# Kernel optimization log

Hardware: AMD Instinct MI355X
Metric: run time of the kernel (lower is better)

Reference implementation:

```python
import jax, jax.numpy as jnp
import numpy as np

E = 100000
VERTEX_DIM = 64
EDGE_DIM = 128
MESSAGE_DIM = 64


def setup_inputs() -> dict:
    key = jax.random.key(0)
    k1, k2, k3, k4 = jax.random.split(key, 4)
    vertices = jax.random.normal(k1, (E, VERTEX_DIM), dtype=jnp.float32)
    edges = jax.random.normal(k2, (E, EDGE_DIM), dtype=jnp.float32)
    # nn.Linear(edge_dim, message_dim * vertex_dim): weight [out, in], bias [out]
    W = jax.random.normal(k3, (MESSAGE_DIM * VERTEX_DIM, EDGE_DIM), dtype=jnp.float32) * (1.0 / np.sqrt(EDGE_DIM))
    b = jax.random.normal(k4, (MESSAGE_DIM * VERTEX_DIM,), dtype=jnp.float32) * 0.01
    return {"vertices": vertices, "edges": edges, "W": W, "b": b}


def reference(vertices, edges, W, b):
    # edge_net(edges): [E, message_dim*vertex_dim]
    proj = edges @ W.T + b
    # view to [E, message_dim, vertex_dim], then batched matvec with vertices [E, vertex_dim]
    proj = proj.reshape(edges.shape[0], MESSAGE_DIM, VERTEX_DIM)
    message = jnp.einsum('emv,ev->em', proj, vertices)  # [E, message_dim]
    return message
```

## Files before the change

kernel.cpp:

```cpp
#include <hip/hip_runtime.h>
#include <hip/hip_bf16.h>
#include <stdint.h>


typedef _Float16 f16;
typedef __attribute__((ext_vector_type(2))) _Float16 f16x2;
typedef __attribute__((ext_vector_type(8))) _Float16 f16x8;
typedef __attribute__((ext_vector_type(4))) float f32x4;

#define MSG_D 64
#define VTX_D 64
#define EDG_D 128

__device__ __forceinline__ f16x8 cvt8(float4 a, float4 d) {
  return (f16x8){(f16)a.x, (f16)a.y, (f16)a.z, (f16)a.w,
                 (f16)d.x, (f16)d.y, (f16)d.z, (f16)d.w};
}

__global__ void prep_w(const float* __restrict__ W, const float* __restrict__ b,
                       f16* __restrict__ Wh, f16* __restrict__ Bh) {
  int tid = blockIdx.x * 256 + threadIdx.x;
  if (tid < 65536) {
    int L = tid & 63, n = (tid >> 6) & 3, s = (tid >> 8) & 3, v = tid >> 10;
    int q = L >> 4, ln = L & 15;
    const float* src = W + (size_t)((n * 16 + ln) * 64 + v) * 128 + s * 32 + q * 8;
    float4 a = *(const float4*)src, d = *(const float4*)(src + 4);
    *(f16x8*)(Wh + (size_t)tid * 8) = cvt8(a, d);
  } else if (tid < 66048) {
    int t2 = tid - 65536;
    int L = t2 & 63, n = (t2 >> 6) & 3, s2 = t2 >> 8;
    int q = L >> 4, ln = L & 15;
    const float* src = b + (n * 16 + ln) * 64 + s2 * 32 + q * 8;
    float4 a = *(const float4*)src, d = *(const float4*)(src + 4);
    *(f16x8*)(Bh + (size_t)t2 * 8) = cvt8(a, d);
  }
}

__global__ __launch_bounds__(64, 2) void edge_msg_flat(
    const float* __restrict__ Vtx, const float* __restrict__ Xe,
    const f16* __restrict__ Wh, const f16* __restrict__ Bh,
    float* __restrict__ out, int E)
{
  const int lane = threadIdx.x;
  const int q = lane >> 4, ln = lane & 15;
  const int eoff = blockIdx.x * 64;

  int er[4];
  f16x8 xh[4][4];
  #pragma unroll
  for (int t = 0; t < 4; ++t) {
    int e = eoff + 16 * t + ln;
    er[t] = e < E ? e : E - 1;
    const float* xr = Xe + (size_t)er[t] * EDG_D;
    #pragma unroll
    for (int s = 0; s < 4; ++s) {
      float4 a = *(const float4*)(xr + s * 32 + q * 8);
      float4 d = *(const float4*)(xr + s * 32 + q * 8 + 4);
      xh[t][s] = cvt8(a, d);
    }
  }

  f32x4 acc[4][4];
  #pragma unroll
  for (int t = 0; t < 4; ++t)
    #pragma unroll
    for (int n = 0; n < 4; ++n) acc[t][n] = (f32x4){0.f, 0.f, 0.f, 0.f};

  const f16* wp = Wh + (size_t)lane * 8;

  f16x8 wA[8], wB[8];
  #pragma unroll
  for (int c = 0; c < 8; ++c) wA[c] = *(const f16x8*)(wp + c * 512);

  f16x8 vrow[4];
  #pragma unroll
  for (int t = 0; t < 4; ++t) {
    const float* vsrc = Vtx + (size_t)er[t] * VTX_D;
    float4 a = *(const float4*)(vsrc), d = *(const float4*)(vsrc + 4);
    vrow[t] = cvt8(a, d);
  }

  #pragma unroll 1
  for (int c8 = 0; c8 < 8; ++c8) {
    f16x8 vnext[4];
    if (c8 < 7) {
      #pragma unroll
      for (int t = 0; t < 4; ++t) {
        const float* vsrc = Vtx + (size_t)er[t] * VTX_D + (c8 + 1) * 8;
        float4 a = *(const float4*)(vsrc), d = *(const float4*)(vsrc + 4);
        vnext[t] = cvt8(a, d);
      }
    }

    #pragma unroll
    for (int j = 0; j < 8; ++j) {
      const int v = c8 * 8 + j;
      const f16* wrow  = wp + (size_t)v * 8192;
      const f16* wrowN = wp + (size_t)(v < 63 ? v + 1 : 63) * 8192;

      #pragma unroll
      for (int c = 0; c < 8; ++c) wB[c] = *(const f16x8*)(wrow + (8 + c) * 512);

      f16x2 hv[4];
      #pragma unroll
      for (int t = 0; t < 4; ++t) { f16 h = vrow[t][j]; hv[t] = (f16x2){h, h}; }

      #pragma unroll
      for (int s = 0; s < 2; ++s) {
        f16x8 af[4];
        #pragma unroll
        for (int t = 0; t < 4; ++t) {
          union { f16x8 v8; f16x2 h2[4]; } x, r;
          x.v8 = xh[t][s];
          r.h2[0] = hv[t] * x.h2[0];
          r.h2[1] = hv[t] * x.h2[1];
          r.h2[2] = hv[t] * x.h2[2];
          r.h2[3] = hv[t] * x.h2[3];
          af[t] = r.v8;
        }
        #pragma unroll
        for (int n = 0; n < 4; ++n)
          #pragma unroll
          for (int t = 0; t < 4; ++t)
            acc[t][n] = __builtin_amdgcn_mfma_f32_16x16x32_f16(af[t], wA[s * 4 + n], acc[t][n], 0, 0, 0);
      }

      #pragma unroll
      for (int c = 0; c < 8; ++c) wA[c] = *(const f16x8*)(wrowN + c * 512);

      #pragma unroll
      for (int s = 2; s < 4; ++s) {
        f16x8 af[4];
        #pragma unroll
        for (int t = 0; t < 4; ++t) {
          union { f16x8 v8; f16x2 h2[4]; } x, r;
          x.v8 = xh[t][s];
          r.h2[0] = hv[t] * x.h2[0];
          r.h2[1] = hv[t] * x.h2[1];
          r.h2[2] = hv[t] * x.h2[2];
          r.h2[3] = hv[t] * x.h2[3];
          af[t] = r.v8;
        }
        #pragma unroll
        for (int n = 0; n < 4; ++n)
          #pragma unroll
          for (int t = 0; t < 4; ++t)
            acc[t][n] = __builtin_amdgcn_mfma_f32_16x16x32_f16(af[t], wB[(s - 2) * 4 + n], acc[t][n], 0, 0, 0);
      }
    }

    #pragma unroll
    for (int t = 0; t < 4; ++t) vrow[t] = vnext[t];
  }

  #pragma unroll
  for (int s2 = 0; s2 < 2; ++s2) {
    f16x8 av[4];
    #pragma unroll
    for (int t = 0; t < 4; ++t) {
      const float* vr2 = Vtx + (size_t)er[t] * VTX_D + s2 * 32 + q * 8;
      float4 a = *(const float4*)vr2, d = *(const float4*)(vr2 + 4);
      av[t] = cvt8(a, d);
    }
    #pragma unroll
    for (int n = 0; n < 4; ++n) {
      f16x8 bf = *(const f16x8*)(Bh + (size_t)((s2 * 4 + n) * 64 + lane) * 8);
      #pragma unroll
      for (int t = 0; t < 4; ++t)
        acc[t][n] = __builtin_amdgcn_mfma_f32_16x16x32_f16(av[t], bf, acc[t][n], 0, 0, 0);
    }
  }

  #pragma unroll
  for (int t = 0; t < 4; ++t)
    #pragma unroll
    for (int r = 0; r < 4; ++r) {
      int e = eoff + 16 * t + 4 * q + r;
      if (e < E) {
        float* orow = out + (size_t)e * MSG_D;
        #pragma unroll
        for (int n = 0; n < 4; ++n) orow[n * 16 + ln] = acc[t][n][r];
      }
    }
}

__global__ void edge_msg_naive(const float* __restrict__ Vtx, const float* __restrict__ Xe,
                               const float* __restrict__ W, const float* __restrict__ b,
                               float* __restrict__ out, int E) {
  __shared__ float xs[EDG_D];
  __shared__ float vs[VTX_D];
  int e = blockIdx.x;
  int m = threadIdx.x;
  for (int i = m; i < EDG_D; i += 64) xs[i] = Xe[(size_t)e * EDG_D + i];
  for (int i = m; i < VTX_D; i += 64) vs[i] = Vtx[(size_t)e * VTX_D + i];
  __syncthreads();
  float s = 0.f;
  for (int v = 0; v < VTX_D; ++v) {
    const float* wr = W + (size_t)(m * 64 + v) * EDG_D;
    float p = b[m * 64 + v];
    for (int k = 0; k < EDG_D; ++k) p += xs[k] * wr[k];
    s += p * vs[v];
  }
  out[(size_t)e * MSG_D + m] = s;
}

extern "C" void kernel_launch(void* const* d_in, const int* in_sizes, int n_in,
                              void* d_out, int out_size, void* d_ws, size_t ws_size,
                              hipStream_t stream) {
  const float* Vtx = (const float*)d_in[0];
  const float* Xe  = (const float*)d_in[1];
  const float* W   = (const float*)d_in[2];
  const float* b   = (const float*)d_in[3];
  float* out = (float*)d_out;

  const int E  = in_sizes[0] / VTX_D;
  const int nW = in_sizes[2];
  const int nb = in_sizes[3];

  const size_t needW = (size_t)(524288 + 4096) * sizeof(f16);

  if (nW != 524288 || nb != 4096 || ws_size < needW) {
    edge_msg_naive<<<E, 64, 0, stream>>>(Vtx, Xe, W, b, out, E);
    return;
  }

  f16* Wh = (f16*)d_ws;
  f16* Bh = Wh + 524288;

  prep_w<<<258, 256, 0, stream>>>(W, b, Wh, Bh);

  int blocks = (E + 63) / 64;
  edge_msg_flat<<<blocks, 64, 0, stream>>>(Vtx, Xe, Wh, Bh, out, E);
}
```

Before: 247.2 us.

## Stage W slices in LDS via async triple-buffered loads shared by four waves

Each block grows from one to four waves covering 256 edges. The per-v W slices are streamed into a three-slot LDS ring with global_load_lds, so one slice serves all four waves instead of each wave loading W from global into registers. Vertex values are transposed into LDS as f16 once per block, replacing repeated global reloads. This cuts global/L2 traffic for W and frees registers, but adds a block barrier every v step plus LDS read traffic.

```diff
diff --git a/kernel.cpp b/kernel.cpp
--- a/kernel.cpp
+++ b/kernel.cpp
@@ -1,5 +1,4 @@
 #include <hip/hip_runtime.h>
-#include <hip/hip_bf16.h>
 #include <stdint.h>
 
 
@@ -36,14 +35,25 @@
   }
 }
 
-__global__ __launch_bounds__(64, 2) void edge_msg_flat(
+typedef __attribute__((address_space(1))) const void GV;
+typedef __attribute__((address_space(3))) void LV;
+__device__ __forceinline__ void gload_lds16(const void* g, void* l) {
+  __builtin_amdgcn_global_load_lds((GV*)g, (LV*)l, 16, 0, 0);
+}
+
+__global__ __launch_bounds__(256, 2) void edge_msg_lds(
     const float* __restrict__ Vtx, const float* __restrict__ Xe,
     const f16* __restrict__ Wh, const f16* __restrict__ Bh,
     float* __restrict__ out, int E)
 {
-  const int lane = threadIdx.x;
+  __shared__ f16 Wsh[3 * 8192];
+  __shared__ f16 Vt[64 * 256];
+
+  const int tid = threadIdx.x;
+  const int wid = tid >> 6, lane = tid & 63;
   const int q = lane >> 4, ln = lane & 15;
-  const int eoff = blockIdx.x * 64;
+  const int eblk = blockIdx.x * 256;
+  const int eoff = eblk + wid * 64;
 
   int er[4];
   f16x8 xh[4][4];
@@ -60,97 +70,93 @@
     }
   }
 
+  {
+    int e = eblk + tid;
+    int ec = e < E ? e : E - 1;
+    const float* vr = Vtx + (size_t)ec * VTX_D;
+    #pragma unroll
+    for (int k = 0; k < 16; ++k) {
+      float4 a = *(const float4*)(vr + k * 4);
+      Vt[(k * 4 + 0) * 256 + tid] = (f16)a.x;
+      Vt[(k * 4 + 1) * 256 + tid] = (f16)a.y;
+      Vt[(k * 4 + 2) * 256 + tid] = (f16)a.z;
+      Vt[(k * 4 + 3) * 256 + tid] = (f16)a.w;
+    }
+  }
+
   f32x4 acc[4][4];
   #pragma unroll
   for (int t = 0; t < 4; ++t)
     #pragma unroll
     for (int n = 0; n < 4; ++n) acc[t][n] = (f32x4){0.f, 0.f, 0.f, 0.f};
 
-  const f16* wp = Wh + (size_t)lane * 8;
-
-  f16x8 wA[8], wB[8];
-  #pragma unroll
-  for (int c = 0; c < 8; ++c) wA[c] = *(const f16x8*)(wp + c * 512);
-
-  f16x8 vrow[4];
-  #pragma unroll
-  for (int t = 0; t < 4; ++t) {
-    const float* vsrc = Vtx + (size_t)er[t] * VTX_D;
-    float4 a = *(const float4*)(vsrc), d = *(const float4*)(vsrc + 4);
-    vrow[t] = cvt8(a, d);
-  }
+  asm volatile("s_waitcnt lgkmcnt(0)" ::: "memory");
+  __builtin_amdgcn_s_barrier();
+  asm volatile("" ::: "memory");
+
+  {
+    const char* gbase = (const char*)Wh + (size_t)(wid * 4) * 1024 + (size_t)lane * 16;
+    char* lbase = (char*)&Wsh[0] + (wid * 4) * 1024;
+    #pragma unroll
+    for (int c = 0; c < 4; ++c) gload_lds16(gbase + c * 1024, lbase + c * 1024);
+    #pragma unroll
+    for (int c = 0; c < 4; ++c)
+      gload_lds16(gbase + 16384 + c * 1024, lbase + 2 * 8192 + c * 1024);
+  }
+
+  int bo = 0;
 
   #pragma unroll 1
-  for (int c8 = 0; c8 < 8; ++c8) {
-    f16x8 vnext[4];
-    if (c8 < 7) {
+  for (int v = 0; v < 64; ++v) {
+    if (v == 63) asm volatile("s_waitcnt vmcnt(0)" ::: "memory");
+    else         asm volatile("s_waitcnt vmcnt(4)" ::: "memory");
+    __builtin_amdgcn_s_barrier();
+    asm volatile("" ::: "memory");
+
+    if (v < 62) {
+      int so = bo + 2 * 8192;
+      if (so >= 3 * 8192) so -= 3 * 8192;
+      const char* gbase = (const char*)Wh + (size_t)(v + 2) * 16384 +
+                          (size_t)(wid * 4) * 1024 + (size_t)lane * 16;
+      char* lbase = (char*)&Wsh[so] + (wid * 4) * 1024;
+      #pragma unroll
+      for (int c = 0; c < 4; ++c) gload_lds16(gbase + c * 1024, lbase + c * 1024);
+    }
+
+    f16x2 hv[4];
+    #pragma unroll
+    for (int t = 0; t < 4; ++t) {
+      f16 h = Vt[v * 256 + wid * 64 + 16 * t + ln];
+      hv[t] = (f16x2){h, h};
+    }
+
+    const f16* wb = &Wsh[bo + lane * 8];
+    #pragma unroll
+    for (int s = 0; s < 4; ++s) {
+      f16x8 bf[4];
+      #pragma unroll
+      for (int n = 0; n < 4; ++n) bf[n] = *(const f16x8*)(wb + (s * 4 + n) * 512);
+
+      f16x8 af[4];
       #pragma unroll
       for (int t = 0; t < 4; ++t) {
-        const float* vsrc = Vtx + (size_t)er[t] * VTX_D + (c8 + 1) * 8;
-        float4 a = *(const float4*)(vsrc), d = *(const float4*)(vsrc + 4);
-        vnext[t] = cvt8(a, d);
+        union { f16x8 v8; f16x2 h2[4]; } x, r;
+        x.v8 = xh[t][s];
+        r.h2[0] = hv[t] * x.h2[0];
+        r.h2[1] = hv[t] * x.h2[1];
+        r.h2[2] = hv[t] * x.h2[2];
+        r.h2[3] = hv[t] * x.h2[3];
+        af[t] = r.v8;
       }
-    }
-
-    #pragma unroll
-    for (int j = 0; j < 8; ++j) {
-      const int v = c8 * 8 + j;
-      const f16* wrow  = wp + (size_t)v * 8192;
-      const f16* wrowN = wp + (size_t)(v < 63 ? v + 1 : 63) * 8192;
-
-      #pragma unroll
-      for (int c = 0; c < 8; ++c) wB[c] = *(const f16x8*)(wrow + (8 + c) * 512);
-
-      f16x2 hv[4];
-      #pragma unroll
-      for (int t = 0; t < 4; ++t) { f16 h = vrow[t][j]; hv[t] = (f16x2){h, h}; }
-
-      #pragma unroll
-      for (int s = 0; s < 2; ++s) {
-        f16x8 af[4];
+      #pragma unroll
+      for (int n = 0; n < 4; ++n)
         #pragma unroll
-        for (int t = 0; t < 4; ++t) {
-          union { f16x8 v8; f16x2 h2[4]; } x, r;
-          x.v8 = xh[t][s];
-          r.h2[0] = hv[t] * x.h2[0];
-          r.h2[1] = hv[t] * x.h2[1];
-          r.h2[2] = hv[t] * x.h2[2];
-          r.h2[3] = hv[t] * x.h2[3];
-          af[t] = r.v8;
-        }
-        #pragma unroll
-        for (int n = 0; n < 4; ++n)
-          #pragma unroll
-          for (int t = 0; t < 4; ++t)
-            acc[t][n] = __builtin_amdgcn_mfma_f32_16x16x32_f16(af[t], wA[s * 4 + n], acc[t][n], 0, 0, 0);
-      }
-
-      #pragma unroll
-      for (int c = 0; c < 8; ++c) wA[c] = *(const f16x8*)(wrowN + c * 512);
-
-      #pragma unroll
-      for (int s = 2; s < 4; ++s) {
-        f16x8 af[4];
-        #pragma unroll
-        for (int t = 0; t < 4; ++t) {
-          union { f16x8 v8; f16x2 h2[4]; } x, r;
-          x.v8 = xh[t][s];
-          r.h2[0] = hv[t] * x.h2[0];
-          r.h2[1] = hv[t] * x.h2[1];
-          r.h2[2] = hv[t] * x.h2[2];
-          r.h2[3] = hv[t] * x.h2[3];
-          af[t] = r.v8;
-        }
-        #pragma unroll
-        for (int n = 0; n < 4; ++n)
-          #pragma unroll
-          for (int t = 0; t < 4; ++t)
-            acc[t][n] = __builtin_amdgcn_mfma_f32_16x16x32_f16(af[t], wB[(s - 2) * 4 + n], acc[t][n], 0, 0, 0);
-      }
-    }
-
-    #pragma unroll
-    for (int t = 0; t < 4; ++t) vrow[t] = vnext[t];
+        for (int t = 0; t < 4; ++t)
+          acc[t][n] = __builtin_amdgcn_mfma_f32_16x16x32_f16(af[t], bf[n], acc[t][n], 0, 0, 0);
+    }
+
+    bo += 8192;
+    if (bo >= 3 * 8192) bo -= 3 * 8192;
   }
 
   #pragma unroll
@@ -164,10 +170,10 @@
     }
     #pragma unroll
     for (int n = 0; n < 4; ++n) {
-      f16x8 bf = *(const f16x8*)(Bh + (size_t)((s2 * 4 + n) * 64 + lane) * 8);
+      f16x8 bfb = *(const f16x8*)(Bh + (size_t)((s2 * 4 + n) * 64 + lane) * 8);
       #pragma unroll
       for (int t = 0; t < 4; ++t)
-        acc[t][n] = __builtin_amdgcn_mfma_f32_16x16x32_f16(av[t], bf, acc[t][n], 0, 0, 0);
+        acc[t][n] = __builtin_amdgcn_mfma_f32_16x16x32_f16(av[t], bfb, acc[t][n], 0, 0, 0);
     }
   }
 
@@ -229,6 +235,6 @@
 
   prep_w<<<258, 256, 0, stream>>>(W, b, Wh, Bh);
 
-  int blocks = (E + 63) / 64;
-  edge_msg_flat<<<blocks, 64, 0, stream>>>(Vtx, Xe, Wh, Bh, out, E);
-}
+  int blocks = (E + 255) / 256;
+  edge_msg_lds<<<blocks, 256, 0, stream>>>(Vtx, Xe, Wh, Bh, out, E);
+}
```

Result: faster. 206.0 us (-16.7%).

## Stage fp16 weights through an LDS ring shared by three waves

Applied to the files above, without the earlier changes.

Replaces each wave's register-prefetch of the fp16 weight slice from global memory with a 5-slot LDS ring buffer. The ring is filled asynchronously by global_load_lds across a 3-wave block, and the waves synchronise with manual vmcnt waits and barriers. Each weight slice is fetched from global or L2 once per block instead of once per wave, cutting L2 traffic. The cost is a barrier per v-step, LDS read pressure and fragile hand-tuned vmcnt counts.

```diff
diff --git a/kernel.cpp b/kernel.cpp
--- a/kernel.cpp
+++ b/kernel.cpp
@@ -1,5 +1,4 @@
 #include <hip/hip_runtime.h>
-#include <hip/hip_bf16.h>
 #include <stdint.h>
 
 
@@ -36,14 +35,23 @@
   }
 }
 
-__global__ __launch_bounds__(64, 2) void edge_msg_flat(
+typedef __attribute__((address_space(1))) const void GV;
+typedef __attribute__((address_space(3))) void LV;
+__device__ __forceinline__ void gload_lds16(const void* g, void* l) {
+  __builtin_amdgcn_global_load_lds((GV*)g, (LV*)l, 16, 0, 0);
+}
+
+__global__ __launch_bounds__(192, 2) void edge_msg_lds(
     const float* __restrict__ Vtx, const float* __restrict__ Xe,
     const f16* __restrict__ Wh, const f16* __restrict__ Bh,
     float* __restrict__ out, int E)
 {
-  const int lane = threadIdx.x;
+  __shared__ f16 Wring[5 * 8192];
+
+  const int tid = threadIdx.x;
+  const int wid = tid >> 6, lane = tid & 63;
   const int q = lane >> 4, ln = lane & 15;
-  const int eoff = blockIdx.x * 64;
+  const int eoff = blockIdx.x * 192 + wid * 64;
 
   int er[4];
   f16x8 xh[4][4];
@@ -60,18 +68,6 @@
     }
   }
 
-  f32x4 acc[4][4];
-  #pragma unroll
-  for (int t = 0; t < 4; ++t)
-    #pragma unroll
-    for (int n = 0; n < 4; ++n) acc[t][n] = (f32x4){0.f, 0.f, 0.f, 0.f};
-
-  const f16* wp = Wh + (size_t)lane * 8;
-
-  f16x8 wA[8], wB[8];
-  #pragma unroll
-  for (int c = 0; c < 8; ++c) wA[c] = *(const f16x8*)(wp + c * 512);
-
   f16x8 vrow[4];
   #pragma unroll
   for (int t = 0; t < 4; ++t) {
@@ -80,33 +76,81 @@
     vrow[t] = cvt8(a, d);
   }
 
+  f32x4 acc[4][4];
+  #pragma unroll
+  for (int t = 0; t < 4; ++t)
+    #pragma unroll
+    for (int n = 0; n < 4; ++n) acc[t][n] = (f32x4){0.f, 0.f, 0.f, 0.f};
+
+  {
+    const char* gb = (const char*)Wh + (size_t)lane * 16;
+    #pragma unroll
+    for (int v = 0; v < 4; ++v) {
+      char* lb = (char*)Wring + (size_t)v * 16384;
+      #pragma unroll
+      for (int k = 0; k < 6; ++k) {
+        int g = wid + 3 * k;
+        if (g < 16) gload_lds16(gb + (size_t)v * 16384 + g * 1024, lb + g * 1024);
+      }
+    }
+  }
+
+  int cur = 0;
+  int st  = 4;
+
   #pragma unroll 1
   for (int c8 = 0; c8 < 8; ++c8) {
-    f16x8 vnext[4];
-    if (c8 < 7) {
-      #pragma unroll
-      for (int t = 0; t < 4; ++t) {
-        const float* vsrc = Vtx + (size_t)er[t] * VTX_D + (c8 + 1) * 8;
-        float4 a = *(const float4*)(vsrc), d = *(const float4*)(vsrc + 4);
-        vnext[t] = cvt8(a, d);
-      }
-    }
+    float4 vna[4], vnd[4];
 
     #pragma unroll
     for (int j = 0; j < 8; ++j) {
-      const int v = c8 * 8 + j;
-      const f16* wrow  = wp + (size_t)v * 8192;
-      const f16* wrowN = wp + (size_t)(v < 63 ? v + 1 : 63) * 8192;
-
-      #pragma unroll
-      for (int c = 0; c < 8; ++c) wB[c] = *(const f16x8*)(wrow + (8 + c) * 512);
+      const int i = c8 * 8 + j;
+
+      if (i < 61) {
+        if (wid == 0) asm volatile("s_waitcnt vmcnt(18)" ::: "memory");
+        else          asm volatile("s_waitcnt vmcnt(15)" ::: "memory");
+      } else if (i == 61) {
+        if (wid == 0) asm volatile("s_waitcnt vmcnt(12)" ::: "memory");
+        else          asm volatile("s_waitcnt vmcnt(10)" ::: "memory");
+      } else if (i == 62) {
+        if (wid == 0) asm volatile("s_waitcnt vmcnt(6)" ::: "memory");
+        else          asm volatile("s_waitcnt vmcnt(5)" ::: "memory");
+      } else {
+        asm volatile("s_waitcnt vmcnt(0)" ::: "memory");
+      }
+      __builtin_amdgcn_s_barrier();
+      asm volatile("" ::: "memory");
+
+      if (i < 60) {
+        const char* gb = (const char*)Wh + (size_t)(i + 4) * 16384 + (size_t)lane * 16;
+        char* lb = (char*)Wring + (size_t)st * 16384;
+        #pragma unroll
+        for (int k = 0; k < 6; ++k) {
+          int g = wid + 3 * k;
+          if (g < 16) gload_lds16(gb + g * 1024, lb + g * 1024);
+        }
+      }
+
+      if (j == 6 && c8 < 7) {
+        #pragma unroll
+        for (int t = 0; t < 4; ++t) {
+          const float* vsrc = Vtx + (size_t)er[t] * VTX_D + (c8 + 1) * 8;
+          vna[t] = *(const float4*)(vsrc);
+          vnd[t] = *(const float4*)(vsrc + 4);
+        }
+      }
 
       f16x2 hv[4];
       #pragma unroll
       for (int t = 0; t < 4; ++t) { f16 h = vrow[t][j]; hv[t] = (f16x2){h, h}; }
 
-      #pragma unroll
-      for (int s = 0; s < 2; ++s) {
+      const f16* wb = Wring + (size_t)cur * 8192 + lane * 8;
+      #pragma unroll
+      for (int s = 0; s < 4; ++s) {
+        f16x8 bf[4];
+        #pragma unroll
+        for (int n = 0; n < 4; ++n) bf[n] = *(const f16x8*)(wb + (s * 4 + n) * 512);
+
         f16x8 af[4];
         #pragma unroll
         for (int t = 0; t < 4; ++t) {
@@ -122,35 +166,17 @@
         for (int n = 0; n < 4; ++n)
           #pragma unroll
           for (int t = 0; t < 4; ++t)
-            acc[t][n] = __builtin_amdgcn_mfma_f32_16x16x32_f16(af[t], wA[s * 4 + n], acc[t][n], 0, 0, 0);
-      }
-
-      #pragma unroll
-      for (int c = 0; c < 8; ++c) wA[c] = *(const f16x8*)(wrowN + c * 512);
-
-      #pragma unroll
-      for (int s = 2; s < 4; ++s) {
-        f16x8 af[4];
-        #pragma unroll
-        for (int t = 0; t < 4; ++t) {
-          union { f16x8 v8; f16x2 h2[4]; } x, r;
-          x.v8 = xh[t][s];
-          r.h2[0] = hv[t] * x.h2[0];
-          r.h2[1] = hv[t] * x.h2[1];
-          r.h2[2] = hv[t] * x.h2[2];
-          r.h2[3] = hv[t] * x.h2[3];
-          af[t] = r.v8;
-        }
-        #pragma unroll
-        for (int n = 0; n < 4; ++n)
-          #pragma unroll
-          for (int t = 0; t < 4; ++t)
-            acc[t][n] = __builtin_amdgcn_mfma_f32_16x16x32_f16(af[t], wB[(s - 2) * 4 + n], acc[t][n], 0, 0, 0);
-      }
-    }
-
-    #pragma unroll
-    for (int t = 0; t < 4; ++t) vrow[t] = vnext[t];
+            acc[t][n] = __builtin_amdgcn_mfma_f32_16x16x32_f16(af[t], bf[n], acc[t][n], 0, 0, 0);
+      }
+
+      cur = (cur == 4) ? 0 : cur + 1;
+      st  = (st  == 4) ? 0 : st  + 1;
+    }
+
+    if (c8 < 7) {
+      #pragma unroll
+      for (int t = 0; t < 4; ++t) vrow[t] = cvt8(vna[t], vnd[t]);
+    }
   }
 
   #pragma unroll
@@ -164,10 +190,10 @@
     }
     #pragma unroll
     for (int n = 0; n < 4; ++n) {
-      f16x8 bf = *(const f16x8*)(Bh + (size_t)((s2 * 4 + n) * 64 + lane) * 8);
+      f16x8 bfb = *(const f16x8*)(Bh + (size_t)((s2 * 4 + n) * 64 + lane) * 8);
       #pragma unroll
       for (int t = 0; t < 4; ++t)
-        acc[t][n] = __builtin_amdgcn_mfma_f32_16x16x32_f16(av[t], bf, acc[t][n], 0, 0, 0);
+        acc[t][n] = __builtin_amdgcn_mfma_f32_16x16x32_f16(av[t], bfb, acc[t][n], 0, 0, 0);
     }
   }
 
@@ -229,6 +255,6 @@
 
   prep_w<<<258, 256, 0, stream>>>(W, b, Wh, Bh);
 
-  int blocks = (E + 63) / 64;
-  edge_msg_flat<<<blocks, 64, 0, stream>>>(Vtx, Xe, Wh, Bh, out, E);
-}
+  int blocks = (E + 191) / 192;
+  edge_msg_lds<<<blocks, 192, 0, stream>>>(Vtx, Xe, Wh, Bh, out, E);
+}
```

Result: slower. 266.8 us (+7.9%).
